# Performance work log

Measured on AMD Instinct MI355X. Metric: run time of the kernel, lower is better.

## Reference

```python
import jax, jax.numpy as jnp
import numpy as np

N1 = 8192; N2 = 8192; E = 131072
D_IN = 128; H = 256; T = 32; B = 16
GCN_DIMS = [(D_IN, H), (H, H), (H, H)]


def _gcn_conv(x, edge_index, W):
    # PyG GCNConv (bias=False): add self-loops, symmetric D^-1/2 (A+I) D^-1/2 normalization.
    n = x.shape[0]
    h = x @ W
    loop = jnp.arange(n, dtype=edge_index.dtype)
    src = jnp.concatenate([edge_index[0], loop])
    dst = jnp.concatenate([edge_index[1], loop])
    deg = jax.ops.segment_sum(jnp.ones(dst.shape[0], h.dtype), dst, num_segments=n)
    dinv = jnp.where(deg > 0, jax.lax.rsqrt(deg), 0.0)
    norm = dinv[src] * dinv[dst]
    return jax.ops.segment_sum(norm[:, None] * h[src], dst, num_segments=n)


def _layer(f1, f2, ei1, ei2, Wg, Wu, bu, last):
    c1 = _gcn_conv(f1, ei1, Wg)
    c2 = _gcn_conv(f2, ei2, Wg)
    sim = f1 @ f2.T                      # [N1, N2] 'dot' similarity
    a1 = jax.nn.softmax(sim, axis=1)     # row softmax
    a2 = jax.nn.softmax(sim, axis=0)     # col softmax
    att1 = a1 @ f2                       # [N1, d]
    att2 = a2.T @ f1                     # [N2, d]
    g1 = jnp.concatenate([c1, f1, f1 - att1], axis=1) @ Wu + bu
    g2 = jnp.concatenate([c2, f2, f2 - att2], axis=1) @ Wu + bu
    if last:
        return g1, g2                    # last layer: no tanh, no dropout
    return jnp.tanh(g1), jnp.tanh(g2)    # dropout is a no-op in eval mode


def _forward(f1, f2, ei1, ei2, avg_v, gcn_Ws, upd_Ws, upd_bs,
             gated_W, gated_b, tn_W, tn_Wb, tn_b, fc1_W, fc1_b, sc_W, sc_b):
    n_layers = len(gcn_Ws)
    for i in range(n_layers):
        f1, f2 = _layer(f1, f2, ei1, ei2, gcn_Ws[i], upd_Ws[i], upd_bs[i],
                        last=(i == n_layers - 1))
    # gated readout: sum(sigmoid(gated(x)) * x)
    p1 = jnp.sum(jax.nn.sigmoid(f1 @ gated_W + gated_b) * f1, axis=0)  # [H]
    p2 = jnp.sum(jax.nn.sigmoid(f2 @ gated_W + gated_b) * f2, axis=0)  # [H]
    # NTN (TensorNetworkModule)
    scoring = jnp.einsum('i,ijt,j->t', p1, tn_W, p2)                   # bilinear term [T]
    block = tn_Wb @ jnp.concatenate([p1, p2])                          # [T]
    ntn = jax.nn.relu(scoring + block + tn_b)
    s = jnp.tanh(ntn @ fc1_W + fc1_b)                                  # [B]
    score = jax.nn.sigmoid(s @ sc_W + sc_b)                            # [1]
    pre_ged = -jnp.log(score) * avg_v                                  # target_mode='exp'
    return score.reshape(-1), pre_ged.reshape(-1)


def setup_inputs():
    key = jax.random.key(0)
    ks = jax.random.split(key, 32)
    rn = lambda k, sh, s=0.05: jax.random.normal(k, sh, dtype=jnp.float32) * s
    inp = {
        'features_1': jax.random.normal(ks[0], (N1, D_IN), dtype=jnp.float32),
        'features_2': jax.random.normal(ks[1], (N2, D_IN), dtype=jnp.float32),
        'edge_index_1': jax.random.randint(ks[2], (2, E), 0, N1, dtype=jnp.int32),
        'edge_index_2': jax.random.randint(ks[3], (2, E), 0, N2, dtype=jnp.int32),
        'avg_v': jnp.full((1,), 12.0, dtype=jnp.float32),
    }
    for i, (di, do) in enumerate(GCN_DIMS):
        inp[f'gcn_W{i}'] = rn(ks[4 + i], (di, do))
        inp[f'upd_W{i}'] = rn(ks[8 + i], (2 * di + do, do))
        inp[f'upd_b{i}'] = jnp.zeros((do,), jnp.float32)
    inp['gated_W'] = rn(ks[12], (H, H)); inp['gated_b'] = jnp.zeros((H,), jnp.float32)
    inp['tn_W'] = rn(ks[13], (H, H, T))
    inp['tn_Wb'] = rn(ks[14], (T, 2 * H)); inp['tn_b'] = jnp.zeros((T,), jnp.float32)
    inp['fc1_W'] = rn(ks[15], (T, B)); inp['fc1_b'] = jnp.zeros((B,), jnp.float32)
    inp['sc_W'] = rn(ks[16], (B, 1)); inp['sc_b'] = jnp.zeros((1,), jnp.float32)
    return inp


def reference(features_1, features_2, edge_index_1, edge_index_2, avg_v,
              gcn_W0, gcn_W1, gcn_W2, upd_W0, upd_W1, upd_W2,
              upd_b0, upd_b1, upd_b2, gated_W, gated_b,
              tn_W, tn_Wb, tn_b, fc1_W, fc1_b, sc_W, sc_b):
    return _forward(features_1, features_2, edge_index_1, edge_index_2, avg_v,
                    [gcn_W0, gcn_W1, gcn_W2], [upd_W0, upd_W1, upd_W2],
                    [upd_b0, upd_b1, upd_b2], gated_W, gated_b,
                    tn_W, tn_Wb, tn_b, fc1_W, fc1_b, sc_W, sc_b)
```

## Files before the change

### kernel.cpp

```cpp
#include <hip/hip_runtime.h>
#include <hip/hip_bf16.h>
#include <stdint.h>

#define NN 8192
#define EDG 131072
#define NSPLIT 4

typedef __attribute__((ext_vector_type(8))) short bf16x8;
typedef __attribute__((ext_vector_type(4))) float f32x4;
typedef unsigned short us;

__device__ __forceinline__ us f2bf(float f) {
  union { float f; unsigned u; } v; v.f = f;
  return (us)((v.u + 0x7fffu + ((v.u >> 16) & 1u)) >> 16);
}

__device__ __forceinline__ us f2bf_trunc(float f) {
  union { float f; unsigned u; } v; v.f = f;
  return (us)(v.u >> 16);
}

__device__ __forceinline__ float bf2f(us u) {
  union { unsigned u; float f; } v; v.u = ((unsigned)u) << 16;
  return v.f;
}

__device__ __forceinline__ void load_lds16(const void* g, void* l) {
  __builtin_amdgcn_global_load_lds(
      (__attribute__((address_space(1))) void*)(uintptr_t)g,
      (__attribute__((address_space(3))) void*)(uintptr_t)l,
      16, 0, 0);
}

template <int EPI>
__global__ __launch_bounds__(256) void gemm_k(
    const us* __restrict__ A, int lda, const us* __restrict__ Bt, int ldb,
    const float* __restrict__ bias, void* __restrict__ Cv, int ldc, int K) {
  __shared__ alignas(16) us As[64 * 32];
  __shared__ alignas(16) us Bs[128 * 32];
  const int t = threadIdx.x;
  const int wave = t >> 6, lane = t & 63;
  const int wrow = wave * 16;
  const int lrow = lane & 15, quad = lane >> 4;
  const int rowBase = blockIdx.x * 64;
  const int colBase = blockIdx.y * 128;
  const int sr = t >> 2, sch = t & 3;

  f32x4 acc[8];
#pragma unroll
  for (int j = 0; j < 8; j++) acc[j] = f32x4{0.f, 0.f, 0.f, 0.f};

  for (int kb = 0; kb < K; kb += 32) {
    __syncthreads();
    const us* asrc = A + (size_t)(rowBase + sr) * lda + kb + sch * 8;
    load_lds16(asrc, (char*)As + t * 16);
    const us* bsrc = Bt + (size_t)(colBase + sr) * ldb + kb + sch * 8;
    load_lds16(bsrc, (char*)Bs + t * 16);
    load_lds16(bsrc + (size_t)64 * ldb, (char*)Bs + t * 16 + 4096);
    __syncthreads();
    bf16x8 af = *(const bf16x8*)&As[(wrow + lrow) * 32 + quad * 8];
#pragma unroll
    for (int j = 0; j < 8; j++) {
      bf16x8 bfr = *(const bf16x8*)&Bs[(j * 16 + lrow) * 32 + quad * 8];
      acc[j] = __builtin_amdgcn_mfma_f32_16x16x32_bf16(af, bfr, acc[j], 0, 0, 0);
    }
  }

#pragma unroll
  for (int j = 0; j < 8; j++) {
    int col = colBase + j * 16 + lrow;
#pragma unroll
    for (int r = 0; r < 4; r++) {
      int row = rowBase + wrow + quad * 4 + r;
      size_t idx = (size_t)row * ldc + col;
      float v = acc[j][r];
      if (EPI == 0) ((float*)Cv)[idx] = v;
      else if (EPI == 2) ((float*)Cv)[idx] = v + bias[col];
      else if (EPI == 4) ((us*)Cv)[idx] = f2bf(v + bias[col]);
      else ((us*)Cv)[idx] = f2bf(tanhf(v + bias[col]));
    }
  }
}

template <int DIN>
__global__ __launch_bounds__(256, (DIN == 128) ? 3 : 2) void flash_att(
    const us* __restrict__ Q, const us* __restrict__ K,
    const us* __restrict__ Vt, us* __restrict__ Opart,
    float* __restrict__ mpart, float* __restrict__ lpart, int kvPerSplit) {
  constexpr int NKC = DIN / 32;
  constexpr int OJ = DIN / 16;
  __shared__ alignas(16) us As[2][64 * 32];
  __shared__ alignas(16) us KB[2][128 * 32];
  __shared__ alignas(16) us Vs[2][DIN * 32];
  us* Ps = &KB[0][0];

  const int t = threadIdx.x;
  const int wave = t >> 6, lane = t & 63;
  const int wrow = wave * 16;
  const int lrow = lane & 15, quad = lane >> 4;
  const int rowBase = blockIdx.x * 64;
  const int split = blockIdx.y;
  const int kv0 = split * kvPerSplit;
  const int sr = t >> 2, sch = t & 3;
  const int pkey = ((lrow >> 2) ^ lrow) & 3;

  auto stageQ = [&](int kc, int buf) {
    const us* qsrc = Q + (size_t)(rowBase + sr) * DIN + kc * 32 + sch * 8;
    load_lds16(qsrc, (char*)&As[buf][0] + t * 16);
  };
  auto stageK = [&](int kt, int kc, int buf) {
    const us* ksrc = K + (size_t)(kt + sr) * DIN + kc * 32 + sch * 8;
    load_lds16(ksrc, (char*)&KB[buf][0] + t * 16);
    load_lds16(ksrc + (size_t)64 * DIN, (char*)&KB[buf][0] + t * 16 + 4096);
  };
  auto stageV = [&](int kt, int cc, int buf) {
#pragma unroll
    for (int p = 0; p < DIN / 64; p++) {
      const us* vsrc = Vt + (size_t)(p * 64 + sr) * NN + kt + cc * 32 + sch * 8;
      load_lds16(vsrc, (char*)&Vs[buf][0] + p * 4096 + t * 16);
    }
  };

  stageQ(0, 0);
  stageV(kv0, 0, 0);

  float m_i[4], l_i[4];
#pragma unroll
  for (int r = 0; r < 4; r++) { m_i[r] = -3.0e38f; l_i[r] = 0.f; }
  f32x4 accO[OJ];
#pragma unroll
  for (int j = 0; j < OJ; j++) accO[j] = f32x4{0.f, 0.f, 0.f, 0.f};

  for (int kt = kv0; kt < kv0 + kvPerSplit; kt += 128) {
    __syncthreads();
    stageK(kt, 0, 0);

    f32x4 accS[8];
#pragma unroll
    for (int j = 0; j < 8; j++) accS[j] = f32x4{0.f, 0.f, 0.f, 0.f};
    for (int kc = 0; kc < NKC; kc++) {
      const int buf = kc & 1;
      __syncthreads();
      if (kc + 1 < NKC) { stageK(kt, kc + 1, buf ^ 1); stageQ(kc + 1, buf ^ 1); }
      bf16x8 af = *(const bf16x8*)&As[buf][(wrow + lrow) * 32 + quad * 8];
#pragma unroll
      for (int j = 0; j < 8; j++) {
        bf16x8 bfr = *(const bf16x8*)&KB[buf][(j * 16 + lrow) * 32 + quad * 8];
        accS[j] = __builtin_amdgcn_mfma_f32_16x16x32_bf16(af, bfr, accS[j], 0, 0, 0);
      }
    }

    float alpha[4];
#pragma unroll
    for (int r = 0; r < 4; r++) {
      float v = accS[0][r];
#pragma unroll
      for (int j = 1; j < 8; j++) v = fmaxf(v, accS[j][r]);
#pragma unroll
      for (int mask = 1; mask < 16; mask <<= 1) v = fmaxf(v, __shfl_xor(v, mask));
      float mn = fmaxf(m_i[r], v);
      alpha[r] = __expf(m_i[r] - mn);
      m_i[r] = mn;
    }
    __syncthreads();
    float ts[4] = {0.f, 0.f, 0.f, 0.f};
#pragma unroll
    for (int j = 0; j < 8; j++)
#pragma unroll
      for (int r = 0; r < 4; r++) {
        float p = __expf(accS[j][r] - m_i[r]);
        ts[r] += p;
        int prow = wrow + quad * 4 + r;
        int key = (quad ^ r) & 3;
        int g = (j * 16 + lrow) >> 3;
        Ps[prow * 128 + ((g ^ (key << 1)) << 3) + (lrow & 7)] = f2bf_trunc(p);
      }
#pragma unroll
    for (int r = 0; r < 4; r++) {
      float v = ts[r];
#pragma unroll
      for (int mask = 1; mask < 16; mask <<= 1) v += __shfl_xor(v, mask);
      l_i[r] = l_i[r] * alpha[r] + v;
    }
#pragma unroll
    for (int j = 0; j < OJ; j++)
#pragma unroll
      for (int r = 0; r < 4; r++) accO[j][r] *= alpha[r];

    const bool hasNext = (kt + 128 < kv0 + kvPerSplit);
    for (int cc = 0; cc < 4; cc++) {
      if (cc) __syncthreads();
      if (cc + 1 < 4) stageV(kt, cc + 1, (cc + 1) & 1);
      else if (hasNext) { stageV(kt + 128, 0, 0); stageQ(0, 0); }
      const int gk = cc * 4 + quad;
      bf16x8 af = *(const bf16x8*)&Ps[(wrow + lrow) * 128 + ((gk ^ (pkey << 1)) << 3)];
      const us* vb = &Vs[cc & 1][0];
#pragma unroll
      for (int j = 0; j < OJ; j++) {
        bf16x8 bfr = *(const bf16x8*)&vb[(j * 16 + lrow) * 32 + quad * 8];
        accO[j] = __builtin_amdgcn_mfma_f32_16x16x32_bf16(af, bfr, accO[j], 0, 0, 0);
      }
    }
  }

#pragma unroll
  for (int j = 0; j < OJ; j++)
#pragma unroll
    for (int r = 0; r < 4; r++) {
      int row = rowBase + wrow + quad * 4 + r;
      int col = j * 16 + lrow;
      Opart[((size_t)split * NN + row) * DIN + col] = f2bf(accO[j][r]);
    }
  if (lrow == 0) {
#pragma unroll
    for (int r = 0; r < 4; r++) {
      int row = rowBase + wrow + quad * 4 + r;
      mpart[(size_t)split * NN + row] = m_i[r];
      lpart[(size_t)split * NN + row] = l_i[r];
    }
  }
}

__global__ void merge_cat(const us* __restrict__ Op, const float* __restrict__ mp,
                          const float* __restrict__ lp, const float* __restrict__ cbuf,
                          const us* __restrict__ fbf, us* __restrict__ cat,
                          int din, int W) {
  int i = blockIdx.y;
  int c = blockIdx.x * 256 + threadIdx.x;
  us o;
  if (c < 256) {
    o = f2bf(cbuf[(size_t)i * 256 + c]);
  } else if (c < 256 + din) {
    o = fbf[(size_t)i * din + (c - 256)];
  } else {
    int f = c - 256 - din;
    float m[NSPLIT], w[NSPLIT];
    float M = -3.0e38f;
#pragma unroll
    for (int s = 0; s < NSPLIT; s++) { m[s] = mp[(size_t)s * NN + i]; M = fmaxf(M, m[s]); }
    float L = 0.f;
#pragma unroll
    for (int s = 0; s < NSPLIT; s++) { w[s] = __expf(m[s] - M); L += lp[(size_t)s * NN + i] * w[s]; }
    float a = 0.f;
#pragma unroll
    for (int s = 0; s < NSPLIT; s++)
      a += w[s] * bf2f(Op[((size_t)s * NN + i) * din + f]);
    o = f2bf(bf2f(fbf[(size_t)i * din + f]) - a / L);
  }
  cat[(size_t)i * W + c] = o;
}


__global__ void ws_sentinel(float* out) { out[0] = 12345.0f; out[1] = 12345.0f; }

__global__ void cvt_bf16(const float* __restrict__ in, us* __restrict__ out, int n) {
  int i = (blockIdx.x * 256 + threadIdx.x) * 4;
  if (i < n) {
    f32x4 v = *(const f32x4*)(in + i);
    uint2 p;
    p.x = f2bf(v.x) | ((unsigned)f2bf(v.y) << 16);
    p.y = f2bf(v.z) | ((unsigned)f2bf(v.w) << 16);
    *(uint2*)(out + i) = p;
  }
}

__global__ void transpose_bf16(const float* __restrict__ src, us* __restrict__ dst,
                               int R, int C) {
  __shared__ float tile[32][33];
  int c0 = blockIdx.x * 32, r0 = blockIdx.y * 32;
  int x = threadIdx.x, y = threadIdx.y;
  for (int i = y; i < 32; i += 8) tile[i][x] = src[(size_t)(r0 + i) * C + c0 + x];
  __syncthreads();
  for (int i = y; i < 32; i += 8) dst[(size_t)(c0 + i) * R + r0 + x] = f2bf(tile[x][i]);
}

__global__ void transpose_bb(const us* __restrict__ src, us* __restrict__ dst,
                             int R, int C) {
  __shared__ us tile[32][33];
  int c0 = blockIdx.x * 32, r0 = blockIdx.y * 32;
  int x = threadIdx.x, y = threadIdx.y;
  for (int i = y; i < 32; i += 8) tile[i][x] = src[(size_t)(r0 + i) * C + c0 + x];
  __syncthreads();
  for (int i = y; i < 32; i += 8) dst[(size_t)(c0 + i) * R + r0 + x] = tile[x][i];
}

__global__ void deg_count(const int* __restrict__ dst, int* __restrict__ deg) {
  int e = blockIdx.x * 256 + threadIdx.x;
  atomicAdd(&deg[dst[e]], 1);
}

__global__ void make_dinv(const int* __restrict__ deg, float* __restrict__ dinv) {
  int v = blockIdx.x * 256 + threadIdx.x;
  dinv[v] = rsqrtf((float)(deg[v] + 1));
}

__global__ void scan_deg(const int* __restrict__ deg, int* __restrict__ rowstart) {
  __shared__ int part[1024];
  int t = threadIdx.x;
  int base = t * 8;
  int local[8];
  int s = 0;
#pragma unroll
  for (int i = 0; i < 8; i++) { local[i] = s; s += deg[base + i]; }
  part[t] = s;
  __syncthreads();
  for (int off = 1; off < 1024; off <<= 1) {
    int v = (t >= off) ? part[t - off] : 0;
    __syncthreads();
    part[t] += v;
    __syncthreads();
  }
  int offset = (t == 0) ? 0 : part[t - 1];
#pragma unroll
  for (int i = 0; i < 8; i++) rowstart[base + i] = offset + local[i];
  if (t == 1023) rowstart[8192] = offset + s;
}

__global__ void csr_fill(const int* __restrict__ src, const int* __restrict__ dst,
                         int* __restrict__ cursor, int* __restrict__ csr_src) {
  int e = blockIdx.x * 256 + threadIdx.x;
  int pos = atomicAdd(&cursor[dst[e]], 1);
  csr_src[pos] = src[e];
}

__global__ __launch_bounds__(256) void gcn_agg(
    const int* __restrict__ rowstart, const int* __restrict__ csr_src,
    const float* __restrict__ dinv, const float* __restrict__ h,
    float* __restrict__ c) {
  int node = blockIdx.x * 4 + (threadIdx.x >> 6);
  int lane = threadIdx.x & 63;
  float dn = dinv[node];
  f32x4 acc = *(const f32x4*)(h + (size_t)node * 256 + lane * 4);
  float w0 = dn * dn;
  acc.x *= w0; acc.y *= w0; acc.z *= w0; acc.w *= w0;
  int s0 = rowstart[node], s1 = rowstart[node + 1];
  for (int j = s0; j < s1; j++) {
    int s = csr_src[j];
    float w = dinv[s] * dn;
    f32x4 v = *(const f32x4*)(h + (size_t)s * 256 + lane * 4);
    acc.x += w * v.x; acc.y += w * v.y; acc.z += w * v.z; acc.w += w * v.w;
  }
  *(f32x4*)(c + (size_t)node * 256 + lane * 4) = acc;
}

__global__ void gated_pool(const float* __restrict__ q, const us* __restrict__ f,
                           float* __restrict__ p) {
  int col = threadIdx.x;
  int r0 = blockIdx.x * 128;
  float a = 0.f;
  for (int i = r0; i < r0 + 128; i++) {
    float qv = q[(size_t)i * 256 + col];
    a += bf2f(f[(size_t)i * 256 + col]) / (1.f + __expf(-qv));
  }
  atomicAdd(&p[col], a);
}

__global__ void ntn_bilinear(const float* __restrict__ p1, const float* __restrict__ tnW,
                             float* __restrict__ tmp) {
  int c = blockIdx.x * 256 + threadIdx.x;
  float a = 0.f;
#pragma unroll 8
  for (int i = 0; i < 256; i++) a += p1[i] * tnW[(size_t)i * 8192 + c];
  tmp[c] = a;
}

__global__ void ntn_final(const float* __restrict__ tmp, const float* __restrict__ p1,
                          const float* __restrict__ p2, const float* __restrict__ tnWb,
                          const float* __restrict__ tnb, const float* __restrict__ fc1W,
                          const float* __restrict__ fc1b, const float* __restrict__ scW,
                          const float* __restrict__ scb, const float* __restrict__ avgv,
                          float* __restrict__ out) {
  __shared__ float pc[512];
  __shared__ float ntn[32];
  __shared__ float sarr[16];
  int t = threadIdx.x;
  pc[t] = p1[t];
  pc[256 + t] = p2[t];
  __syncthreads();
  if (t < 32) {
    float sc = 0.f;
    for (int j = 0; j < 256; j++) sc += tmp[j * 32 + t] * pc[256 + j];
    float bl = 0.f;
    for (int k = 0; k < 512; k++) bl += tnWb[t * 512 + k] * pc[k];
    float v = sc + bl + tnb[t];
    ntn[t] = v > 0.f ? v : 0.f;
  }
  __syncthreads();
  if (t < 16) {
    float a = fc1b[t];
    for (int i = 0; i < 32; i++) a += ntn[i] * fc1W[i * 16 + t];
    sarr[t] = tanhf(a);
  }
  __syncthreads();
  if (t == 0) {
    float a = scb[0];
    for (int b = 0; b < 16; b++) a += sarr[b] * scW[b];
    float score = 1.f / (1.f + expf(-a));
    out[0] = score;
    out[1] = -logf(score) * avgv[0];
  }
}


extern "C" void kernel_launch(void* const* d_in, const int* in_sizes, int n_in,
                              void* d_out, int out_size, void* d_ws, size_t ws_size,
                              hipStream_t stream) {
  (void)in_sizes; (void)n_in; (void)out_size;
  const float* feat1 = (const float*)d_in[0];
  const float* feat2 = (const float*)d_in[1];
  const int* ei1 = (const int*)d_in[2];
  const int* ei2 = (const int*)d_in[3];
  const float* avgv = (const float*)d_in[4];
  const float* gcnW[3] = {(const float*)d_in[5], (const float*)d_in[8], (const float*)d_in[11]};
  const float* updW[3] = {(const float*)d_in[6], (const float*)d_in[9], (const float*)d_in[12]};
  const float* updb[3] = {(const float*)d_in[7], (const float*)d_in[10], (const float*)d_in[13]};
  const float* gatedW = (const float*)d_in[14];
  const float* gatedb = (const float*)d_in[15];
  const float* tnW = (const float*)d_in[16];
  const float* tnWb = (const float*)d_in[17];
  const float* tnb = (const float*)d_in[18];
  const float* fc1W = (const float*)d_in[19];
  const float* fc1b = (const float*)d_in[20];
  const float* scW = (const float*)d_in[21];
  const float* scb = (const float*)d_in[22];
  float* out = (float*)d_out;

  char* wp = (char*)d_ws;
  auto take = [&](size_t b) { char* p = wp; wp += (b + 255) & ~(size_t)255; return p; };
  us* Op = (us*)take((size_t)NSPLIT * NN * 256 * 2);
  us* cat1 = (us*)take((size_t)NN * 768 * 2);
  us* cat2 = (us*)take((size_t)NN * 768 * 2);
  us* fA1 = (us*)take((size_t)NN * 256 * 2);
  us* fA2 = (us*)take((size_t)NN * 256 * 2);
  us* fB1 = (us*)take((size_t)NN * 256 * 2);
  us* fB2 = (us*)take((size_t)NN * 256 * 2);
  us* f1bT = (us*)take((size_t)NN * 256 * 2);
  us* f2bT = (us*)take((size_t)NN * 256 * 2);
  float* h1 = (float*)take((size_t)NN * 256 * 4);
  float* h2 = (float*)take((size_t)NN * 256 * 4);
  float* c1 = (float*)take((size_t)NN * 256 * 4);
  float* c2 = (float*)take((size_t)NN * 256 * 4);
  us* WgT[3], *WuT[3];
  for (int l = 0; l < 3; l++) WgT[l] = (us*)take(256 * 256 * 2);
  for (int l = 0; l < 3; l++) WuT[l] = (us*)take(256 * 768 * 2);
  us* gWT = (us*)take(256 * 256 * 2);
  int* deg1 = (int*)take(NN * 4);
  int* deg2 = (int*)take(NN * 4);
  float* dinv1 = (float*)take(NN * 4);
  float* dinv2 = (float*)take(NN * 4);
  int* rs1 = (int*)take((NN + 1) * 4);
  int* rs2 = (int*)take((NN + 1) * 4);
  int* cur1 = (int*)take(NN * 4);
  int* cur2 = (int*)take(NN * 4);
  int* csr1 = (int*)take((size_t)EDG * 4);
  int* csr2 = (int*)take((size_t)EDG * 4);
  float* mp = (float*)take((size_t)NSPLIT * NN * 4);
  float* lp = (float*)take((size_t)NSPLIT * NN * 4);
  float* p1 = (float*)take(1024);
  float* p2 = (float*)take(1024);
  float* tmp = (float*)take(NN * 4);

  size_t need = (size_t)(wp - (char*)d_ws);
  if (need > ws_size) {
    ws_sentinel<<<1, 1, 0, stream>>>(out);
    return;
  }

  hipMemsetAsync(deg1, 0, NN * 4, stream);
  hipMemsetAsync(deg2, 0, NN * 4, stream);
  deg_count<<<EDG / 256, 256, 0, stream>>>(ei1 + EDG, deg1);
  deg_count<<<EDG / 256, 256, 0, stream>>>(ei2 + EDG, deg2);
  make_dinv<<<NN / 256, 256, 0, stream>>>(deg1, dinv1);
  make_dinv<<<NN / 256, 256, 0, stream>>>(deg2, dinv2);
  scan_deg<<<1, 1024, 0, stream>>>(deg1, rs1);
  scan_deg<<<1, 1024, 0, stream>>>(deg2, rs2);
  hipMemcpyAsync(cur1, rs1, NN * 4, hipMemcpyDeviceToDevice, stream);
  hipMemcpyAsync(cur2, rs2, NN * 4, hipMemcpyDeviceToDevice, stream);
  csr_fill<<<EDG / 256, 256, 0, stream>>>(ei1, ei1 + EDG, cur1, csr1);
  csr_fill<<<EDG / 256, 256, 0, stream>>>(ei2, ei2 + EDG, cur2, csr2);

  for (int l = 0; l < 3; l++) {
    int din = (l == 0) ? 128 : 256;
    int W = 256 + 2 * din;
    transpose_bf16<<<dim3(8, din / 32), dim3(32, 8), 0, stream>>>(gcnW[l], WgT[l], din, 256);
    transpose_bf16<<<dim3(8, W / 32), dim3(32, 8), 0, stream>>>(updW[l], WuT[l], W, 256);
  }
  transpose_bf16<<<dim3(8, 8), dim3(32, 8), 0, stream>>>(gatedW, gWT, 256, 256);

  us* f1 = fA1; us* f2 = fA2;
  us* fn1 = fB1; us* fn2 = fB2;
  cvt_bf16<<<NN * 128 / 1024, 256, 0, stream>>>(feat1, f1, NN * 128);
  cvt_bf16<<<NN * 128 / 1024, 256, 0, stream>>>(feat2, f2, NN * 128);

  for (int l = 0; l < 3; l++) {
    const int din = (l == 0) ? 128 : 256;
    const int W = 256 + 2 * din;

    if (l == 0) {
      transpose_bf16<<<dim3(din / 32, NN / 32), dim3(32, 8), 0, stream>>>(feat1, f1bT, NN, din);
      transpose_bf16<<<dim3(din / 32, NN / 32), dim3(32, 8), 0, stream>>>(feat2, f2bT, NN, din);
    } else {
      transpose_bb<<<dim3(din / 32, NN / 32), dim3(32, 8), 0, stream>>>(f1, f1bT, NN, din);
      transpose_bb<<<dim3(din / 32, NN / 32), dim3(32, 8), 0, stream>>>(f2, f2bT, NN, din);
    }

    gemm_k<0><<<dim3(128, 2), 256, 0, stream>>>(f1, din, WgT[l], din, nullptr, h1, 256, din);
    gemm_k<0><<<dim3(128, 2), 256, 0, stream>>>(f2, din, WgT[l], din, nullptr, h2, 256, din);

    gcn_agg<<<NN / 4, 256, 0, stream>>>(rs1, csr1, dinv1, h1, c1);
    gcn_agg<<<NN / 4, 256, 0, stream>>>(rs2, csr2, dinv2, h2, c2);

    if (l == 0) {
      flash_att<128><<<dim3(NN / 64, NSPLIT), 256, 0, stream>>>(f1, f2, f2bT, Op, mp, lp, NN / NSPLIT);
      merge_cat<<<dim3(W / 256, NN), 256, 0, stream>>>(Op, mp, lp, c1, f1, cat1, din, W);
      flash_att<128><<<dim3(NN / 64, NSPLIT), 256, 0, stream>>>(f2, f1, f1bT, Op, mp, lp, NN / NSPLIT);
      merge_cat<<<dim3(W / 256, NN), 256, 0, stream>>>(Op, mp, lp, c2, f2, cat2, din, W);
    } else {
      flash_att<256><<<dim3(NN / 64, NSPLIT), 256, 0, stream>>>(f1, f2, f2bT, Op, mp, lp, NN / NSPLIT);
      merge_cat<<<dim3(W / 256, NN), 256, 0, stream>>>(Op, mp, lp, c1, f1, cat1, din, W);
      flash_att<256><<<dim3(NN / 64, NSPLIT), 256, 0, stream>>>(f2, f1, f1bT, Op, mp, lp, NN / NSPLIT);
      merge_cat<<<dim3(W / 256, NN), 256, 0, stream>>>(Op, mp, lp, c2, f2, cat2, din, W);
    }

    if (l < 2) {
      gemm_k<5><<<dim3(128, 2), 256, 0, stream>>>(cat1, W, WuT[l], W, updb[l], fn1, 256, W);
      gemm_k<5><<<dim3(128, 2), 256, 0, stream>>>(cat2, W, WuT[l], W, updb[l], fn2, 256, W);
    } else {
      gemm_k<4><<<dim3(128, 2), 256, 0, stream>>>(cat1, W, WuT[l], W, updb[l], fn1, 256, W);
      gemm_k<4><<<dim3(128, 2), 256, 0, stream>>>(cat2, W, WuT[l], W, updb[l], fn2, 256, W);
    }
    us* s;
    s = f1; f1 = fn1; fn1 = s;
    s = f2; f2 = fn2; fn2 = s;
  }

  gemm_k<2><<<dim3(128, 2), 256, 0, stream>>>(f1, 256, gWT, 256, gatedb, c1, 256, 256);
  gemm_k<2><<<dim3(128, 2), 256, 0, stream>>>(f2, 256, gWT, 256, gatedb, c2, 256, 256);
  hipMemsetAsync(p1, 0, 256 * 4, stream);
  hipMemsetAsync(p2, 0, 256 * 4, stream);
  gated_pool<<<64, 256, 0, stream>>>(c1, f1, p1);
  gated_pool<<<64, 256, 0, stream>>>(c2, f2, p2);

  ntn_bilinear<<<32, 256, 0, stream>>>(p1, tnW, tmp);
  ntn_final<<<1, 256, 0, stream>>>(tmp, p1, p2, tnWb, tnb, fc1W, fc1b, scW, scb, avgv, out);
}
```

Before: 1.209 ms.

## Widen flash-attention KV tile to 256 and store GCN intermediates in bf16

The flash-attention kernel now processes 256 keys per iteration instead of 128. It doubles the K staging buffer and score accumulators, halving the per-tile softmax and sync overhead relative to the work done. The GCN path folds the source-side dinv scaling into the GEMM epilogue and writes h and the aggregate as bf16, which halves gather traffic in gcn_agg and lets merge_cat copy bf16 directly. The risks are higher register and LDS pressure, which lowers occupancy for DIN=128 (launch bound 3 becomes 2), and extra rounding from bf16 storage.

```diff
diff --git a/kernel.cpp b/kernel.cpp
--- a/kernel.cpp
+++ b/kernel.cpp
@@ -77,20 +77,21 @@
       if (EPI == 0) ((float*)Cv)[idx] = v;
       else if (EPI == 2) ((float*)Cv)[idx] = v + bias[col];
       else if (EPI == 4) ((us*)Cv)[idx] = f2bf(v + bias[col]);
-      else ((us*)Cv)[idx] = f2bf(tanhf(v + bias[col]));
+      else if (EPI == 5) ((us*)Cv)[idx] = f2bf(tanhf(v + bias[col]));
+      else ((us*)Cv)[idx] = f2bf(v * bias[row]);
     }
   }
 }
 
 template <int DIN>
-__global__ __launch_bounds__(256, (DIN == 128) ? 3 : 2) void flash_att(
+__global__ __launch_bounds__(256, 2) void flash_att(
     const us* __restrict__ Q, const us* __restrict__ K,
     const us* __restrict__ Vt, us* __restrict__ Opart,
     float* __restrict__ mpart, float* __restrict__ lpart, int kvPerSplit) {
   constexpr int NKC = DIN / 32;
   constexpr int OJ = DIN / 16;
   __shared__ alignas(16) us As[2][64 * 32];
-  __shared__ alignas(16) us KB[2][128 * 32];
+  __shared__ alignas(16) us KB[2][256 * 32];
   __shared__ alignas(16) us Vs[2][DIN * 32];
   us* Ps = &KB[0][0];
 
@@ -110,8 +111,9 @@
   };
   auto stageK = [&](int kt, int kc, int buf) {
     const us* ksrc = K + (size_t)(kt + sr) * DIN + kc * 32 + sch * 8;
-    load_lds16(ksrc, (char*)&KB[buf][0] + t * 16);
-    load_lds16(ksrc + (size_t)64 * DIN, (char*)&KB[buf][0] + t * 16 + 4096);
+#pragma unroll
+    for (int p = 0; p < 4; p++)
+      load_lds16(ksrc + (size_t)(p * 64) * DIN, (char*)&KB[buf][0] + p * 4096 + t * 16);
   };
   auto stageV = [&](int kt, int cc, int buf) {
 #pragma unroll
@@ -131,20 +133,20 @@
 #pragma unroll
   for (int j = 0; j < OJ; j++) accO[j] = f32x4{0.f, 0.f, 0.f, 0.f};
 
-  for (int kt = kv0; kt < kv0 + kvPerSplit; kt += 128) {
+  for (int kt = kv0; kt < kv0 + kvPerSplit; kt += 256) {
     __syncthreads();
     stageK(kt, 0, 0);
 
-    f32x4 accS[8];
-#pragma unroll
-    for (int j = 0; j < 8; j++) accS[j] = f32x4{0.f, 0.f, 0.f, 0.f};
+    f32x4 accS[16];
+#pragma unroll
+    for (int j = 0; j < 16; j++) accS[j] = f32x4{0.f, 0.f, 0.f, 0.f};
     for (int kc = 0; kc < NKC; kc++) {
       const int buf = kc & 1;
       __syncthreads();
       if (kc + 1 < NKC) { stageK(kt, kc + 1, buf ^ 1); stageQ(kc + 1, buf ^ 1); }
       bf16x8 af = *(const bf16x8*)&As[buf][(wrow + lrow) * 32 + quad * 8];
 #pragma unroll
-      for (int j = 0; j < 8; j++) {
+      for (int j = 0; j < 16; j++) {
         bf16x8 bfr = *(const bf16x8*)&KB[buf][(j * 16 + lrow) * 32 + quad * 8];
         accS[j] = __builtin_amdgcn_mfma_f32_16x16x32_bf16(af, bfr, accS[j], 0, 0, 0);
       }
@@ -155,7 +157,7 @@
     for (int r = 0; r < 4; r++) {
       float v = accS[0][r];
 #pragma unroll
-      for (int j = 1; j < 8; j++) v = fmaxf(v, accS[j][r]);
+      for (int j = 1; j < 16; j++) v = fmaxf(v, accS[j][r]);
 #pragma unroll
       for (int mask = 1; mask < 16; mask <<= 1) v = fmaxf(v, __shfl_xor(v, mask));
       float mn = fmaxf(m_i[r], v);
@@ -165,15 +167,15 @@
     __syncthreads();
     float ts[4] = {0.f, 0.f, 0.f, 0.f};
 #pragma unroll
-    for (int j = 0; j < 8; j++)
+    for (int j = 0; j < 16; j++)
 #pragma unroll
       for (int r = 0; r < 4; r++) {
         float p = __expf(accS[j][r] - m_i[r]);
         ts[r] += p;
         int prow = wrow + quad * 4 + r;
         int key = (quad ^ r) & 3;
-        int g = (j * 16 + lrow) >> 3;
-        Ps[prow * 128 + ((g ^ (key << 1)) << 3) + (lrow & 7)] = f2bf_trunc(p);
+        int g = 2 * j + (lrow >> 3);
+        Ps[prow * 256 + ((g ^ (key << 1)) << 3) + (lrow & 7)] = f2bf_trunc(p);
       }
 #pragma unroll
     for (int r = 0; r < 4; r++) {
@@ -187,13 +189,13 @@
 #pragma unroll
       for (int r = 0; r < 4; r++) accO[j][r] *= alpha[r];
 
-    const bool hasNext = (kt + 128 < kv0 + kvPerSplit);
-    for (int cc = 0; cc < 4; cc++) {
+    const bool hasNext = (kt + 256 < kv0 + kvPerSplit);
+    for (int cc = 0; cc < 8; cc++) {
       if (cc) __syncthreads();
-      if (cc + 1 < 4) stageV(kt, cc + 1, (cc + 1) & 1);
-      else if (hasNext) { stageV(kt + 128, 0, 0); stageQ(0, 0); }
+      if (cc + 1 < 8) stageV(kt, cc + 1, (cc + 1) & 1);
+      else if (hasNext) { stageV(kt + 256, 0, 0); stageQ(0, 0); }
       const int gk = cc * 4 + quad;
-      bf16x8 af = *(const bf16x8*)&Ps[(wrow + lrow) * 128 + ((gk ^ (pkey << 1)) << 3)];
+      bf16x8 af = *(const bf16x8*)&Ps[(wrow + lrow) * 256 + ((gk ^ (pkey << 1)) << 3)];
       const us* vb = &Vs[cc & 1][0];
 #pragma unroll
       for (int j = 0; j < OJ; j++) {
@@ -222,14 +224,14 @@
 }
 
 __global__ void merge_cat(const us* __restrict__ Op, const float* __restrict__ mp,
-                          const float* __restrict__ lp, const float* __restrict__ cbuf,
+                          const float* __restrict__ lp, const us* __restrict__ cbuf,
                           const us* __restrict__ fbf, us* __restrict__ cat,
                           int din, int W) {
   int i = blockIdx.y;
   int c = blockIdx.x * 256 + threadIdx.x;
   us o;
   if (c < 256) {
-    o = f2bf(cbuf[(size_t)i * 256 + c]);
+    o = cbuf[(size_t)i * 256 + c];
   } else if (c < 256 + din) {
     o = fbf[(size_t)i * din + (c - 256)];
   } else {
@@ -323,24 +325,28 @@
   csr_src[pos] = src[e];
 }
 
-__global__ __launch_bounds__(256) void gcn_agg(
+__global__ __launch_bounds__(256) void gcn_agg_b(
     const int* __restrict__ rowstart, const int* __restrict__ csr_src,
-    const float* __restrict__ dinv, const float* __restrict__ h,
-    float* __restrict__ c) {
+    const float* __restrict__ dinv, const us* __restrict__ hs,
+    us* __restrict__ c) {
   int node = blockIdx.x * 4 + (threadIdx.x >> 6);
   int lane = threadIdx.x & 63;
-  float dn = dinv[node];
-  f32x4 acc = *(const f32x4*)(h + (size_t)node * 256 + lane * 4);
-  float w0 = dn * dn;
-  acc.x *= w0; acc.y *= w0; acc.z *= w0; acc.w *= w0;
+  const us* hp = hs + lane * 4;
+  uint2 u = *(const uint2*)(hp + (size_t)node * 256);
+  float a0 = bf2f(u.x & 0xffffu), a1 = bf2f(u.x >> 16);
+  float a2 = bf2f(u.y & 0xffffu), a3 = bf2f(u.y >> 16);
   int s0 = rowstart[node], s1 = rowstart[node + 1];
   for (int j = s0; j < s1; j++) {
     int s = csr_src[j];
-    float w = dinv[s] * dn;
-    f32x4 v = *(const f32x4*)(h + (size_t)s * 256 + lane * 4);
-    acc.x += w * v.x; acc.y += w * v.y; acc.z += w * v.z; acc.w += w * v.w;
-  }
-  *(f32x4*)(c + (size_t)node * 256 + lane * 4) = acc;
+    uint2 v = *(const uint2*)(hp + (size_t)s * 256);
+    a0 += bf2f(v.x & 0xffffu); a1 += bf2f(v.x >> 16);
+    a2 += bf2f(v.y & 0xffffu); a3 += bf2f(v.y >> 16);
+  }
+  float dn = dinv[node];
+  uint2 o;
+  o.x = f2bf(a0 * dn) | ((unsigned)f2bf(a1 * dn) << 16);
+  o.y = f2bf(a2 * dn) | ((unsigned)f2bf(a3 * dn) << 16);
+  *(uint2*)(c + (size_t)node * 256 + lane * 4) = o;
 }
 
 __global__ void gated_pool(const float* __restrict__ q, const us* __restrict__ f,
@@ -436,10 +442,12 @@
   us* fB2 = (us*)take((size_t)NN * 256 * 2);
   us* f1bT = (us*)take((size_t)NN * 256 * 2);
   us* f2bT = (us*)take((size_t)NN * 256 * 2);
-  float* h1 = (float*)take((size_t)NN * 256 * 4);
-  float* h2 = (float*)take((size_t)NN * 256 * 4);
-  float* c1 = (float*)take((size_t)NN * 256 * 4);
-  float* c2 = (float*)take((size_t)NN * 256 * 4);
+  us* hs1 = (us*)take((size_t)NN * 256 * 2);
+  us* hs2 = (us*)take((size_t)NN * 256 * 2);
+  us* cb1 = (us*)take((size_t)NN * 256 * 2);
+  us* cb2 = (us*)take((size_t)NN * 256 * 2);
+  float* q1 = (float*)take((size_t)NN * 256 * 4);
+  float* q2 = (float*)take((size_t)NN * 256 * 4);
   us* WgT[3], *WuT[3];
   for (int l = 0; l < 3; l++) WgT[l] = (us*)take(256 * 256 * 2);
   for (int l = 0; l < 3; l++) WuT[l] = (us*)take(256 * 768 * 2);
@@ -504,22 +512,22 @@
       transpose_bb<<<dim3(din / 32, NN / 32), dim3(32, 8), 0, stream>>>(f2, f2bT, NN, din);
     }
 
-    gemm_k<0><<<dim3(128, 2), 256, 0, stream>>>(f1, din, WgT[l], din, nullptr, h1, 256, din);
-    gemm_k<0><<<dim3(128, 2), 256, 0, stream>>>(f2, din, WgT[l], din, nullptr, h2, 256, din);
-
-    gcn_agg<<<NN / 4, 256, 0, stream>>>(rs1, csr1, dinv1, h1, c1);
-    gcn_agg<<<NN / 4, 256, 0, stream>>>(rs2, csr2, dinv2, h2, c2);
+    gemm_k<6><<<dim3(128, 2), 256, 0, stream>>>(f1, din, WgT[l], din, dinv1, hs1, 256, din);
+    gemm_k<6><<<dim3(128, 2), 256, 0, stream>>>(f2, din, WgT[l], din, dinv2, hs2, 256, din);
+
+    gcn_agg_b<<<NN / 4, 256, 0, stream>>>(rs1, csr1, dinv1, hs1, cb1);
+    gcn_agg_b<<<NN / 4, 256, 0, stream>>>(rs2, csr2, dinv2, hs2, cb2);
 
     if (l == 0) {
       flash_att<128><<<dim3(NN / 64, NSPLIT), 256, 0, stream>>>(f1, f2, f2bT, Op, mp, lp, NN / NSPLIT);
-      merge_cat<<<dim3(W / 256, NN), 256, 0, stream>>>(Op, mp, lp, c1, f1, cat1, din, W);
+      merge_cat<<<dim3(W / 256, NN), 256, 0, stream>>>(Op, mp, lp, cb1, f1, cat1, din, W);
       flash_att<128><<<dim3(NN / 64, NSPLIT), 256, 0, stream>>>(f2, f1, f1bT, Op, mp, lp, NN / NSPLIT);
-      merge_cat<<<dim3(W / 256, NN), 256, 0, stream>>>(Op, mp, lp, c2, f2, cat2, din, W);
+      merge_cat<<<dim3(W / 256, NN), 256, 0, stream>>>(Op, mp, lp, cb2, f2, cat2, din, W);
     } else {
       flash_att<256><<<dim3(NN / 64, NSPLIT), 256, 0, stream>>>(f1, f2, f2bT, Op, mp, lp, NN / NSPLIT);
-      merge_cat<<<dim3(W / 256, NN), 256, 0, stream>>>(Op, mp, lp, c1, f1, cat1, din, W);
+      merge_cat<<<dim3(W / 256, NN), 256, 0, stream>>>(Op, mp, lp, cb1, f1, cat1, din, W);
       flash_att<256><<<dim3(NN / 64, NSPLIT), 256, 0, stream>>>(f2, f1, f1bT, Op, mp, lp, NN / NSPLIT);
-      merge_cat<<<dim3(W / 256, NN), 256, 0, stream>>>(Op, mp, lp, c2, f2, cat2, din, W);
+      merge_cat<<<dim3(W / 256, NN), 256, 0, stream>>>(Op, mp, lp, cb2, f2, cat2, din, W);
     }
 
     if (l < 2) {
@@ -534,12 +542,12 @@
     s = f2; f2 = fn2; fn2 = s;
   }
 
-  gemm_k<2><<<dim3(128, 2), 256, 0, stream>>>(f1, 256, gWT, 256, gatedb, c1, 256, 256);
-  gemm_k<2><<<dim3(128, 2), 256, 0, stream>>>(f2, 256, gWT, 256, gatedb, c2, 256, 256);
+  gemm_k<2><<<dim3(128, 2), 256, 0, stream>>>(f1, 256, gWT, 256, gatedb, q1, 256, 256);
+  gemm_k<2><<<dim3(128, 2), 256, 0, stream>>>(f2, 256, gWT, 256, gatedb, q2, 256, 256);
   hipMemsetAsync(p1, 0, 256 * 4, stream);
   hipMemsetAsync(p2, 0, 256 * 4, stream);
-  gated_pool<<<64, 256, 0, stream>>>(c1, f1, p1);
-  gated_pool<<<64, 256, 0, stream>>>(c2, f2, p2);
+  gated_pool<<<64, 256, 0, stream>>>(q1, f1, p1);
+  gated_pool<<<64, 256, 0, stream>>>(q2, f2, p2);
 
   ntn_bilinear<<<32, 256, 0, stream>>>(p1, tnW, tmp);
   ntn_final<<<1, 256, 0, stream>>>(tmp, p1, p2, tnWb, tnb, fc1W, fc1b, scW, scb, avgv, out);
```

After: 1.216 ms. No clear change (+0.6%).
